# Performance work log

Measured on AMD Instinct MI355X. Metric: run time of the kernel, lower is better.

The kernel has to match this reference:

```python
import jax, jax.numpy as jnp
import numpy as np
import math

PAD = 0
EPS = 1e-5


def _mha(x, ids, num_heads, qw, qb, kw, kb, vw, vb, pw, pb):
    # Faithful vectorization of the per-head Python loop: identical math per head.
    B, S, D = x.shape
    d = D // num_heads
    q = (x @ qw + qb).reshape(B, S, num_heads, d)
    k = (x @ kw + kb).reshape(B, S, num_heads, d)
    v = (x @ vw + vb).reshape(B, S, num_heads, d)
    scores = jnp.einsum('bqhd,bkhd->bhqk', q, k) / math.sqrt(d)
    key_mask = (ids != PAD)[:, None, None, :]  # mask padded KEYS only (as in source)
    scores = jnp.where(key_mask, scores, -jnp.inf)
    w = jax.nn.softmax(scores, axis=-1)
    out = jnp.einsum('bhqk,bkhd->bqhd', w, v).reshape(B, S, D)
    return out @ pw + pb + x  # projection + residual


def setup_inputs() -> dict:
    V, D, B, S = 50257, 1024, 64, 512
    key = jax.random.key(0)
    ks = jax.random.split(key, 24)
    s = 0.02

    def lin(k, din, dout):
        k1, k2 = jax.random.split(k)
        return (jax.random.normal(k1, (din, dout), jnp.float32) * s,
                jax.random.normal(k2, (dout,), jnp.float32) * s)

    x = jax.random.randint(ks[0], (B, S), 0, V, dtype=jnp.int64)
    emb_w = jax.random.normal(ks[1], (V, D), jnp.float32) * s
    pos_w = jax.random.normal(ks[2], (512, D), jnp.float32) * s
    a1_qw, a1_qb = lin(ks[3], D, D)
    a1_kw, a1_kb = lin(ks[4], D, D)
    a1_vw, a1_vb = lin(ks[5], D, D)
    a1_pw, a1_pb = lin(ks[6], D, D)
    a2_qw, a2_qb = lin(ks[7], D, D)
    a2_kw, a2_kb = lin(ks[8], D, D)
    a2_vw, a2_vb = lin(ks[9], D, D)
    a2_pw, a2_pb = lin(ks[10], D, D)
    norm_g = jnp.ones((D,), jnp.float32)
    norm_b = jnp.zeros((D,), jnp.float32)
    lin_w, lin_b = lin(ks[11], D, 1)
    return dict(x=x, emb_w=emb_w, pos_w=pos_w,
                a1_qw=a1_qw, a1_qb=a1_qb, a1_kw=a1_kw, a1_kb=a1_kb,
                a1_vw=a1_vw, a1_vb=a1_vb, a1_pw=a1_pw, a1_pb=a1_pb,
                a2_qw=a2_qw, a2_qb=a2_qb, a2_kw=a2_kw, a2_kb=a2_kb,
                a2_vw=a2_vw, a2_vb=a2_vb, a2_pw=a2_pw, a2_pb=a2_pb,
                norm_g=norm_g, norm_b=norm_b, lin_w=lin_w, lin_b=lin_b)


def reference(x, emb_w, pos_w,
              a1_qw, a1_qb, a1_kw, a1_kb, a1_vw, a1_vb, a1_pw, a1_pb,
              a2_qw, a2_qb, a2_kw, a2_kb, a2_vw, a2_vb, a2_pw, a2_pb,
              norm_g, norm_b, lin_w, lin_b):
    B, S = x.shape
    h = emb_w[x] + pos_w[jnp.arange(S)][None, :, :]  # word + positional emb
    res_emb = h
    h = _mha(h, x, 8, a1_qw, a1_qb, a1_kw, a1_kb, a1_vw, a1_vb, a1_pw, a1_pb)
    # dropout is identity in eval
    h = _mha(h, x, 4, a2_qw, a2_qb, a2_kw, a2_kb, a2_vw, a2_vb, a2_pw, a2_pb)
    h = h + res_emb
    # mean pooling over non-pad tokens (type=0 branch)
    m = (x != PAD)[:, :, None].astype(h.dtype)
    pooled = jnp.sum(h * m, axis=1) / jnp.sum(m, axis=1)
    # LayerNorm
    mu = jnp.mean(pooled, axis=-1, keepdims=True)
    var = jnp.mean((pooled - mu) ** 2, axis=-1, keepdims=True)
    normed = (pooled - mu) / jnp.sqrt(var + EPS) * norm_g + norm_b
    return normed @ lin_w + lin_b  # [B, 1]
```

## Files before the change

kernel.cpp:

```cpp
#include <hip/hip_runtime.h>

typedef unsigned short u16;
typedef short short8 __attribute__((ext_vector_type(8)));
typedef unsigned short u16x8 __attribute__((ext_vector_type(8)));
typedef float f32x4 __attribute__((ext_vector_type(4)));
typedef const __attribute__((address_space(1))) void* gptr_t;
typedef __attribute__((address_space(3))) void* lptr_t;

#define B_  64
#define S_  512
#define D_  1024
#define BS_ (B_*S_)

__device__ __forceinline__ float b2f(u16 v) {
    union { float f; unsigned u; } c; c.u = ((unsigned)v) << 16; return c.f;
}
__device__ __forceinline__ u16 f2b(float f) {
    union { float f; unsigned u; } c; c.f = f;
    unsigned r = c.u + 0x7FFFu + ((c.u >> 16) & 1u);
    return (u16)(r >> 16);
}

__global__ void detect_k(const u16* __restrict__ raw, int* __restrict__ flag) {
    __shared__ int cnt;
    if (threadIdx.x == 0) cnt = 0;
    __syncthreads();
    u16 v = raw[threadIdx.x * 2];
    int e = (v >> 7) & 0xFF;
    int sane = (e >= 64 && e <= 150) ? 1 : 0;
    atomicAdd(&cnt, sane);
    __syncthreads();
    if (threadIdx.x == 0) *flag = (cnt >= 192) ? 1 : 0;
}

__global__ __launch_bounds__(256) void convert_params_k(
    const void* b0, const void* b1, const void* b2, const void* b3,
    const void* b4, const void* b5, const void* b6, const void* b7,
    const void* g, const void* be, const void* lw, const void* lb,
    const int* __restrict__ flagp, u16* __restrict__ dst)
{
    const void* srcs[12] = {b0, b1, b2, b3, b4, b5, b6, b7, g, be, lw, lb};
    int slot = blockIdx.x;
    int n = (slot == 11) ? 1 : 1024;
    int f = *flagp;
    const void* s = srcs[slot];
    for (int i = threadIdx.x; i < n; i += 256) {
        float v = f ? b2f(((const u16*)s)[i]) : ((const float*)s)[i];
        dst[slot * 1024 + i] = f2b(v);
    }
}

__global__ __launch_bounds__(256) void transpose_all_k(
    const void* w0, const void* w1, const void* w2, const void* w3,
    const void* w4, const void* w5, const void* w6, const void* w7,
    u16* __restrict__ WtBase, const int* __restrict__ flagp) {
    __shared__ float t[32][33];
    const void* srcs[8] = {w0, w1, w2, w3, w4, w5, w6, w7};
    int z = blockIdx.z;
    const void* W = srcs[z];
    u16* Wt = WtBase + (size_t)z * (D_ * D_);
    int f = *flagp;
    int tx = threadIdx.x, ty = threadIdx.y;
    int x0 = blockIdx.x * 32, y0 = blockIdx.y * 32;
    for (int i = ty; i < 32; i += 8) {
        size_t idx = (size_t)(y0 + i) * D_ + x0 + tx;
        t[i][tx] = f ? b2f(((const u16*)W)[idx]) : ((const float*)W)[idx];
    }
    __syncthreads();
    for (int i = ty; i < 32; i += 8)
        Wt[(size_t)(x0 + i) * D_ + y0 + tx] = f2b(t[tx][i]);
}

__global__ __launch_bounds__(256) void embed_k(const int* __restrict__ x, const void* __restrict__ emb,
                                               const void* __restrict__ pos, u16* __restrict__ h0,
                                               const int* __restrict__ flagp) {
    int f = *flagp;
    int bs = blockIdx.x;
    int s = bs & (S_ - 1);
    int tok = x[bs];
    u16* orow = h0 + (size_t)bs * D_;
    int c = threadIdx.x * 4;
    float e0, e1, e2, e3, p0, p1, p2, p3;
    if (f) {
        ushort4 e = *(const ushort4*)((const u16*)emb + (size_t)tok * D_ + c);
        ushort4 p = *(const ushort4*)((const u16*)pos + (size_t)s * D_ + c);
        e0 = b2f(e.x); e1 = b2f(e.y); e2 = b2f(e.z); e3 = b2f(e.w);
        p0 = b2f(p.x); p1 = b2f(p.y); p2 = b2f(p.z); p3 = b2f(p.w);
    } else {
        float4 e = *(const float4*)((const float*)emb + (size_t)tok * D_ + c);
        float4 p = *(const float4*)((const float*)pos + (size_t)s * D_ + c);
        e0 = e.x; e1 = e.y; e2 = e.z; e3 = e.w;
        p0 = p.x; p1 = p.y; p2 = p.z; p3 = p.w;
    }
    ushort4 o;
    o.x = f2b(e0 + p0); o.y = f2b(e1 + p1); o.z = f2b(e2 + p2); o.w = f2b(e3 + p3);
    *(ushort4*)(orow + c) = o;
}

template <int NT>
__global__ __launch_bounds__(512, 2) void gemm256_k(
    const u16* __restrict__ A, const u16* __restrict__ Bt,
    const u16* __restrict__ bias,
    const u16* __restrict__ res, const u16* __restrict__ res2,
    u16* __restrict__ Cq, u16* __restrict__ Ck, u16* __restrict__ Vt,
    const int* __restrict__ xm, float* __restrict__ pool)
{
    int bid = blockIdx.x;
    int xcd = bid & 7;
    int loc = bid >> 3;
    int chunk = loc >> 6;
    int r = loc & 63;
    int mt = xcd * 16 + (r >> 2);
    int nt = chunk * 4 + (r & 3);
    int m0 = mt * 256, n0 = nt * 256;

    int tid = threadIdx.x;
    int lane = tid & 63, wid = tid >> 6, quad = lane >> 4, l16 = lane & 15;
    int wm = wid >> 2, wn = wid & 3;
    int pxor = l16 & 7;

    __shared__ __align__(16) u16 lds[2][2][2][128 * 64];

    f32x4 acc[8][4];
#pragma unroll
    for (int i = 0; i < 8; i++)
#pragma unroll
        for (int j = 0; j < 4; j++) acc[i][j] = (f32x4){0.f, 0.f, 0.f, 0.f};

    int srow = tid >> 3;
    int skof = ((tid & 7) ^ (srow & 7)) * 8;

    auto STAGE_HALF = [&](int kt, int mat, int hlf) {
        int p = kt & 1;
        int kbase = kt * 64;
        const u16* src = (mat == 0)
            ? A  + (size_t)(m0 + hlf * 128) * D_ + kbase
            : Bt + (size_t)(n0 + hlf * 128) * D_ + kbase;
        u16* dst = &lds[p][mat][hlf][0];
        __builtin_amdgcn_global_load_lds((gptr_t)(src + (size_t)srow * D_ + skof),
                                         (lptr_t)(dst + tid * 8), 16, 0, 0);
        __builtin_amdgcn_global_load_lds((gptr_t)(src + (size_t)(srow + 64) * D_ + skof),
                                         (lptr_t)(dst + 4096 + tid * 8), 16, 0, 0);
    };

    STAGE_HALF(0, 0, 0); STAGE_HALF(0, 0, 1);
    STAGE_HALF(0, 1, 0); STAGE_HALF(0, 1, 1);
    STAGE_HALF(1, 1, 0); STAGE_HALF(1, 1, 1);
    asm volatile("s_waitcnt vmcnt(4)" ::: "memory");
    __builtin_amdgcn_s_barrier();

    int brow0 = (wn & 1) * 64;
    for (int kt = 0; kt < 16; ++kt) {
        int p = kt & 1;
        const u16* Ah = &lds[p][0][wm][0];
        const u16* Bh = &lds[p][1][wn >> 1][0];
        short8 bf[4][2];
#pragma unroll
        for (int q = 0; q < 4; ++q) {
            if (q == 0) {
#pragma unroll
                for (int nj = 0; nj < 4; ++nj)
#pragma unroll
                    for (int kh = 0; kh < 2; ++kh)
                        bf[nj][kh] = *(const short8*)&Bh[(brow0 + nj * 16 + l16) * 64 +
                                                         ((kh * 4 + quad) ^ pxor) * 8];
            }
            short8 af[2][2];
#pragma unroll
            for (int mi2 = 0; mi2 < 2; ++mi2)
#pragma unroll
                for (int kh = 0; kh < 2; ++kh)
                    af[mi2][kh] = *(const short8*)&Ah[((2 * q + mi2) * 16 + l16) * 64 +
                                                      ((kh * 4 + quad) ^ pxor) * 8];
            if (q == 0 && kt + 1 < 16) STAGE_HALF(kt + 1, 0, 0);
            if (q == 1 && kt + 1 < 16) STAGE_HALF(kt + 1, 0, 1);
            if (q == 2 && kt + 2 < 16) STAGE_HALF(kt + 2, 1, 0);
            if (q == 3 && kt + 2 < 16) STAGE_HALF(kt + 2, 1, 1);
            __builtin_amdgcn_s_barrier();
            asm volatile("s_waitcnt lgkmcnt(0)" ::: "memory");
            __builtin_amdgcn_sched_barrier(0);
            __builtin_amdgcn_s_setprio(1);
#pragma unroll
            for (int kh = 0; kh < 2; ++kh)
#pragma unroll
                for (int mi2 = 0; mi2 < 2; ++mi2)
#pragma unroll
                    for (int nj = 0; nj < 4; ++nj)
                        acc[2 * q + mi2][nj] = __builtin_amdgcn_mfma_f32_16x16x32_bf16(
                            af[mi2][kh], bf[nj][kh], acc[2 * q + mi2][nj], 0, 0, 0);
            __builtin_amdgcn_s_setprio(0);
            __builtin_amdgcn_s_barrier();
        }
        if (kt < 15) {
            if (kt < 14) asm volatile("s_waitcnt vmcnt(4)" ::: "memory");
            else         asm volatile("s_waitcnt vmcnt(0)" ::: "memory");
            __builtin_amdgcn_s_barrier();
        }
    }

    __syncthreads();
    float* fl = (float*)(&lds[0][0][0][0]) + wid * 1104;

    int nbase = n0 + wn * 64;
    bool vwave = (NT == 12) && (nbase >= 2048);

    if (vwave) {
        int colv = nbase + lane - 2048;
        float bv = b2f(bias[nbase + lane]);
#pragma unroll
        for (int mi = 0; mi < 8; ++mi) {
#pragma unroll
            for (int nj = 0; nj < 4; ++nj)
                *(f32x4*)&fl[(nj * 16 + l16) * 17 + quad * 4] = acc[mi][nj];
            asm volatile("s_waitcnt lgkmcnt(0)" ::: "memory");
            int rowbase = m0 + wm * 128 + mi * 16;
            int bb = rowbase >> 9, sb0 = rowbase & (S_ - 1);
            u16x8 o0, o1;
#pragma unroll
            for (int s = 0; s < 8; ++s) {
                o0[s] = f2b(fl[lane * 17 + s] + bv);
                o1[s] = f2b(fl[lane * 17 + 8 + s] + bv);
            }
            u16* dst = Vt + ((size_t)bb * D_ + colv) * S_ + sb0;
            *(u16x8*)dst = o0;
            *(u16x8*)(dst + 8) = o1;
            asm volatile("" ::: "memory");
        }
    } else {
        u16* Cd = (NT == 12 && nbase >= 1024) ? Ck : Cq;
        int rr2 = lane >> 2, sg = lane & 3;
        float bvv[2][8];
#pragma unroll
        for (int g = 0; g < 2; ++g) {
            u16x8 b8 = *(const u16x8*)&bias[nbase + sg * 8 + g * 32];
#pragma unroll
            for (int j = 0; j < 8; ++j) bvv[g][j] = b2f(b8[j]);
        }
        float psum[2][8];
#pragma unroll
        for (int g = 0; g < 2; ++g)
#pragma unroll
            for (int j = 0; j < 8; ++j) psum[g][j] = 0.f;
        int rowb0 = m0 + wm * 128;
        int b_ = rowb0 >> 9;
        const int* xb_ = pool ? (xm + b_ * S_) : nullptr;

#pragma unroll
        for (int mi = 0; mi < 8; ++mi) {
#pragma unroll
            for (int nj = 0; nj < 4; ++nj)
                *(f32x4*)&fl[(nj * 16 + l16) * 17 + quad * 4] = acc[mi][nj];
            asm volatile("s_waitcnt lgkmcnt(0)" ::: "memory");
            int row_g = rowb0 + mi * 16 + rr2;
            int msk = pool ? (xb_[row_g & (S_ - 1)] != 0) : 0;
#pragma unroll
            for (int g = 0; g < 2; ++g) {
                int c0 = sg * 8 + g * 32;
                int colc = (nbase + c0) & 1023;
                size_t idx = (size_t)row_g * D_ + colc;
                float v[8];
#pragma unroll
                for (int j = 0; j < 8; ++j)
                    v[j] = fl[(c0 + j) * 17 + rr2] + bvv[g][j];
                if (res) {
                    u16x8 r8 = *(const u16x8*)&res[idx];
#pragma unroll
                    for (int j = 0; j < 8; ++j) v[j] += b2f(r8[j]);
                }
                if (res2) {
                    u16x8 r8 = *(const u16x8*)&res2[idx];
#pragma unroll
                    for (int j = 0; j < 8; ++j) v[j] += b2f(r8[j]);
                }
                if (pool) {
                    if (msk)
#pragma unroll
                        for (int j = 0; j < 8; ++j) psum[g][j] += v[j];
                } else {
                    u16x8 o;
#pragma unroll
                    for (int j = 0; j < 8; ++j) o[j] = f2b(v[j]);
                    *(u16x8*)&Cd[idx] = o;
                }
            }
            asm volatile("" ::: "memory");
        }
        if (pool) {
#pragma unroll
            for (int g = 0; g < 2; ++g)
#pragma unroll
                for (int j = 0; j < 8; ++j) {
#pragma unroll
                    for (int m = 4; m <= 32; m <<= 1)
                        psum[g][j] += __shfl_xor(psum[g][j], m, 64);
                }
            if (rr2 == 0) {
#pragma unroll
                for (int g = 0; g < 2; ++g) {
                    int colc = (nbase + sg * 8 + g * 32) & 1023;
#pragma unroll
                    for (int j = 0; j < 8; ++j)
                        atomicAdd(&pool[b_ * 1024 + colc + j], psum[g][j]);
                }
            }
        }
    }
}

template <int HD, int NBUF>
__global__ __launch_bounds__(512, HD == 128 ? 4 : 2) void attn8_k(
    const u16* Q, const u16* __restrict__ Kn, const u16* __restrict__ Vt,
    const int* __restrict__ x, u16* O, int H)
{
    constexpr int NKF = HD / 32, NOF = HD / 16;
    constexpr int KP = HD + 8;
    constexpr int VP = (HD == 256 && NBUF == 2) ? 36 : 40;
    constexpr int KC = (32 * HD / 8) / 512;
    constexpr int VC = (HD * 32 / 8) / 512;
    const float scale = (HD == 128) ? 0.08838834764831845f : 0.0625f;
    int bh = blockIdx.x;
    int b = bh / H, h = bh - b * H;
    int tid = threadIdx.x, wid = tid >> 6, lane = tid & 63, quad = lane >> 4, l16 = lane & 15;
    int qrow = blockIdx.y * 128 + wid * 16;

    const u16* Qb = Q + (size_t)(b * S_) * D_ + h * HD;
    const u16* Kb = Kn + (size_t)(b * S_) * D_ + h * HD;
    const u16* Vb = Vt + ((size_t)b * D_ + h * HD) * S_;
    const int* xb = x + b * S_;

    __shared__ __align__(16) u16 Ks[NBUF][32 * KP];
    __shared__ __align__(16) u16 Vs[NBUF][HD * VP];
    __shared__ __align__(16) u16 Pl[8 * 16 * 32];

    short8 qf[NKF];
#pragma unroll
    for (int f = 0; f < NKF; ++f)
        qf[f] = *(const short8*)(Qb + (size_t)(qrow + l16) * D_ + f * 32 + quad * 8);

    f32x4 of[NOF];
    float lpart[4];
#pragma unroll
    for (int f = 0; f < NOF; ++f) of[f] = (f32x4){0.f, 0.f, 0.f, 0.f};
#pragma unroll
    for (int r = 0; r < 4; ++r) lpart[r] = 0.f;

    short8 kreg[KC], vreg[VC];
    auto LOADKV = [&](int key0) {
#pragma unroll
        for (int i = 0; i < KC; ++i) {
            int c = tid + i * 512;
            int row = c / (HD / 8), col = (c % (HD / 8)) * 8;
            kreg[i] = *(const short8*)(Kb + (size_t)(key0 + row) * D_ + col);
        }
#pragma unroll
        for (int i = 0; i < VC; ++i) {
            int c = tid + i * 512;
            int row = c >> 2, col = (c & 3) * 8;
            vreg[i] = *(const short8*)(Vb + (size_t)row * S_ + key0 + col);
        }
    };

    LOADKV(0);

    for (int t = 0; t < 16; ++t) {
        int key0 = t * 32;
        int p = (NBUF == 2) ? (t & 1) : 0;
        if (NBUF == 1) __syncthreads();
#pragma unroll
        for (int i = 0; i < KC; ++i) {
            int c = tid + i * 512;
            int row = c / (HD / 8), col = (c % (HD / 8)) * 8;
            *(short8*)&Ks[p][row * KP + col] = kreg[i];
        }
#pragma unroll
        for (int i = 0; i < VC; ++i) {
            int c = tid + i * 512;
            int row = c >> 2, col = (c & 3) * 8;
            *(short8*)&Vs[p][row * VP + col] = vreg[i];
        }
        if (key0 + 32 < S_) LOADKV(key0 + 32);
        int tok0 = xb[key0 + l16] != 0;
        int tok1 = xb[key0 + 16 + l16] != 0;
        __syncthreads();

        f32x4 sc0 = (f32x4){0.f, 0.f, 0.f, 0.f};
        f32x4 sc1 = (f32x4){0.f, 0.f, 0.f, 0.f};
#pragma unroll
        for (int f = 0; f < NKF; ++f) {
            short8 k0 = *(const short8*)&Ks[p][l16 * KP + f * 32 + quad * 8];
            short8 k1 = *(const short8*)&Ks[p][(16 + l16) * KP + f * 32 + quad * 8];
            sc0 = __builtin_amdgcn_mfma_f32_16x16x32_bf16(qf[f], k0, sc0, 0, 0, 0);
            sc1 = __builtin_amdgcn_mfma_f32_16x16x32_bf16(qf[f], k1, sc1, 0, 0, 0);
        }
#pragma unroll
        for (int r = 0; r < 4; ++r) {
            float p0 = tok0 ? __expf(sc0[r] * scale) : 0.f;
            float p1 = tok1 ? __expf(sc1[r] * scale) : 0.f;
            lpart[r] += p0 + p1;
            Pl[wid * 512 + (quad * 4 + r) * 32 + l16] = f2b(p0);
            Pl[wid * 512 + (quad * 4 + r) * 32 + 16 + l16] = f2b(p1);
        }
        __asm volatile("s_waitcnt lgkmcnt(0)" ::: "memory");
        short8 pf = *(const short8*)&Pl[wid * 512 + l16 * 32 + quad * 8];
#pragma unroll
        for (int f = 0; f < NOF; ++f) {
            short8 vf = *(const short8*)&Vs[p][(f * 16 + l16) * VP + quad * 8];
            of[f] = __builtin_amdgcn_mfma_f32_16x16x32_bf16(pf, vf, of[f], 0, 0, 0);
        }
    }

    u16* Ob = O + (size_t)(b * S_) * D_ + h * HD;
    float rl[4];
#pragma unroll
    for (int r = 0; r < 4; ++r) {
        float l = lpart[r];
#pragma unroll
        for (int msk = 1; msk < 16; msk <<= 1) l += __shfl_xor(l, msk, 64);
        rl[r] = 1.0f / l;
    }
#pragma unroll
    for (int f = 0; f < NOF; ++f)
#pragma unroll
        for (int r = 0; r < 4; ++r)
            Ob[(size_t)(qrow + quad * 4 + r) * D_ + f * 16 + l16] =
                f2b(of[f][r] * rl[r]);
}

__global__ __launch_bounds__(256) void pool_zero_k(float* __restrict__ pooled) {
    int b = blockIdx.x;
    for (int i = threadIdx.x; i < 1024; i += 256) pooled[b * 1024 + i] = 0.f;
}

__global__ __launch_bounds__(256) void pool_final_k(
    const float* __restrict__ pooled, const int* __restrict__ x,
    const u16* __restrict__ prm, void* __restrict__ out, const int* __restrict__ flagp)
{
    __shared__ float sb[8];
    __shared__ int sbi[4];
    const u16* g  = prm + 8 * 1024;
    const u16* be = prm + 9 * 1024;
    const u16* lw = prm + 10 * 1024;
    const u16* lb = prm + 11 * 1024;
    int b = blockIdx.x;
    int c = threadIdx.x * 4;
    int wid = threadIdx.x >> 6, lane = threadIdx.x & 63;

    const int* xb = x + b * S_;
    int localc = 0;
    for (int i = threadIdx.x; i < S_; i += 256) localc += (xb[i] != 0);
#pragma unroll
    for (int m = 32; m >= 1; m >>= 1) localc += __shfl_xor(localc, m, 64);
    if (lane == 0) sbi[wid] = localc;
    __syncthreads();
    int n = sbi[0] + sbi[1] + sbi[2] + sbi[3];

    float inv = 1.0f / (float)(n > 0 ? n : 1);
    float p0 = pooled[b * 1024 + c + 0] * inv;
    float p1 = pooled[b * 1024 + c + 1] * inv;
    float p2 = pooled[b * 1024 + c + 2] * inv;
    float p3 = pooled[b * 1024 + c + 3] * inv;
    float s1 = p0 + p1 + p2 + p3;
    float s2 = p0 * p0 + p1 * p1 + p2 * p2 + p3 * p3;
#pragma unroll
    for (int m = 32; m >= 1; m >>= 1) { s1 += __shfl_xor(s1, m, 64); s2 += __shfl_xor(s2, m, 64); }
    if (lane == 0) { sb[wid] = s1; sb[4 + wid] = s2; }
    __syncthreads();
    float S1 = sb[0] + sb[1] + sb[2] + sb[3];
    float S2 = sb[4] + sb[5] + sb[6] + sb[7];
    float mu = S1 * (1.0f / 1024.0f);
    float var = S2 * (1.0f / 1024.0f) - mu * mu;
    float rstd = rsqrtf(var + 1e-5f);
    float dot = ((p0 - mu) * rstd * b2f(g[c + 0]) + b2f(be[c + 0])) * b2f(lw[c + 0])
              + ((p1 - mu) * rstd * b2f(g[c + 1]) + b2f(be[c + 1])) * b2f(lw[c + 1])
              + ((p2 - mu) * rstd * b2f(g[c + 2]) + b2f(be[c + 2])) * b2f(lw[c + 2])
              + ((p3 - mu) * rstd * b2f(g[c + 3]) + b2f(be[c + 3])) * b2f(lw[c + 3]);
#pragma unroll
    for (int m = 32; m >= 1; m >>= 1) dot += __shfl_xor(dot, m, 64);
    __syncthreads();
    if (lane == 0) sb[wid] = dot;
    __syncthreads();
    if (threadIdx.x == 0) {
        float v = sb[0] + sb[1] + sb[2] + sb[3] + b2f(lb[0]);
        if (*flagp) ((u16*)out)[b] = f2b(v);
        else        ((float*)out)[b] = v;
    }
}

extern "C" void kernel_launch(void* const* d_in, const int* in_sizes, int n_in,
                              void* d_out, int out_size, void* d_ws, size_t ws_size,
                              hipStream_t stream)
{
    (void)in_sizes; (void)n_in; (void)out_size; (void)ws_size;
    const int* x = (const int*)d_in[0];

    char* ws = (char*)d_ws;
    size_t off = 0;
    auto carve = [&](size_t bytes) -> char* {
        char* p = ws + off;
        off += (bytes + 255) & ~(size_t)255;
        return p;
    };
    int* flag    = (int*)carve(256);
    u16* prm     = (u16*)carve(12 * 1024 * 2);
    float* pooled = (float*)carve(64 * 1024 * 4);
    int* cnt     = (int*)carve(64 * 4);
    (void)cnt;
    const size_t WB = (size_t)D_ * D_ * 2;
    const size_t HB = (size_t)BS_ * D_ * 2;
    u16* wt0 = (u16*)carve(WB * 8);
    u16* h0   = (u16*)carve(HB);
    u16* buf2 = (u16*)carve(HB);
    u16* buf3 = (u16*)carve(HB);
    u16* buf4 = (u16*)carve(HB);
    u16* buf5 = (u16*)carve(HB);
    const size_t WE = (size_t)D_ * D_;

    detect_k<<<1, 256, 0, stream>>>((const u16*)d_in[1], flag);
    convert_params_k<<<12, 256, 0, stream>>>(
        d_in[4], d_in[6], d_in[8], d_in[10], d_in[12], d_in[14], d_in[16], d_in[18],
        d_in[19], d_in[20], d_in[21], d_in[22], flag, prm);

    transpose_all_k<<<dim3(32, 32, 8), dim3(32, 8), 0, stream>>>(
        d_in[3], d_in[5], d_in[7], d_in[9], d_in[11], d_in[13], d_in[15], d_in[17],
        wt0, flag);

    embed_k<<<BS_, 256, 0, stream>>>(x, d_in[1], d_in[2], h0, flag);

    pool_zero_k<<<B_, 256, 0, stream>>>(pooled);

    gemm256_k<12><<<1536, 512, 0, stream>>>(h0, wt0 + 0 * WE, prm + 0 * 1024,
                                            nullptr, nullptr, buf2, buf3, buf4,
                                            nullptr, nullptr);
    attn8_k<128, 2><<<dim3(B_ * 8, 4), 512, 0, stream>>>(buf2, buf3, buf4, x, buf2, 8);
    gemm256_k<4><<<512, 512, 0, stream>>>(buf2, wt0 + 3 * WE, prm + 3 * 1024,
                                          h0, nullptr, buf5, nullptr, nullptr,
                                          nullptr, nullptr);
    gemm256_k<12><<<1536, 512, 0, stream>>>(buf5, wt0 + 4 * WE, prm + 4 * 1024,
                                            nullptr, nullptr, buf2, buf3, buf4,
                                            nullptr, nullptr);
    attn8_k<256, 2><<<dim3(B_ * 4, 4), 512, 0, stream>>>(buf2, buf3, buf4, x, buf2, 4);
    gemm256_k<4><<<512, 512, 0, stream>>>(buf2, wt0 + 7 * WE, prm + 7 * 1024,
                                          buf5, h0, nullptr, nullptr, nullptr,
                                          x, pooled);

    pool_final_k<<<B_, 256, 0, stream>>>(pooled, x, prm, d_out, flag);
}
```

Baseline: 974.2 us.

## Add dedicated 128x256-tile QKV GEMM kernel with higher occupancy

Replaces the 256x256-tile QKV projection GEMM with a new kernel that uses 128x256 tiles, a simpler double-buffered K=32 pipeline, 4x4 accumulators per wave, and launch bounds allowing 4 blocks per CU. It launches 3072 blocks in place of 1536, with an XCD-aware tile mapping. The aim is more occupancy and better load balance for the QKV projection, at the cost of less reuse per tile (more global traffic for B). The V-transpose epilogue moves from the generic GEMM into the new kernel, leaving the old GEMM with only the Q/out-projection path.

```diff
diff --git a/kernel.cpp b/kernel.cpp
--- a/kernel.cpp
+++ b/kernel.cpp
@@ -97,6 +97,140 @@
     *(ushort4*)(orow + c) = o;
 }
 
+__global__ __launch_bounds__(512, 4) void gemmqkv_k(
+    const u16* __restrict__ A, const u16* __restrict__ Bt,
+    const u16* __restrict__ bias,
+    u16* __restrict__ Cq, u16* __restrict__ Ck, u16* __restrict__ Vt)
+{
+    int bid = blockIdx.x;
+    int xcd = bid & 7;
+    int loc = bid >> 3;
+    int chunk = loc >> 7;
+    int r = loc & 127;
+    int mt = xcd * 32 + (r >> 2);
+    int nt = chunk * 4 + (r & 3);
+    int m0 = mt * 128, n0 = nt * 256;
+
+    int tid = threadIdx.x;
+    int lane = tid & 63, wid = tid >> 6, quad = lane >> 4, l16 = lane & 15;
+    int wm = wid >> 2, wn = wid & 3;
+    int pxor = (l16 >> 1) & 3;
+
+    __shared__ __align__(16) u16 lds[2][12288];
+
+    f32x4 acc[4][4];
+#pragma unroll
+    for (int i = 0; i < 4; i++)
+#pragma unroll
+        for (int j = 0; j < 4; j++) acc[i][j] = (f32x4){0.f, 0.f, 0.f, 0.f};
+
+    int srow = tid >> 2;
+    int skof = (((tid & 3) ^ ((tid >> 3) & 3)) * 8);
+
+    auto STAGE = [&](int s) {
+        int p = s & 1;
+        int kbase = s * 32;
+        __builtin_amdgcn_global_load_lds(
+            (gptr_t)(A + (size_t)(m0 + srow) * D_ + kbase + skof),
+            (lptr_t)(&lds[p][0] + tid * 8), 16, 0, 0);
+#pragma unroll
+        for (int l = 0; l < 2; ++l) {
+            int row = l * 128 + srow;
+            __builtin_amdgcn_global_load_lds(
+                (gptr_t)(Bt + (size_t)(n0 + row) * D_ + kbase + skof),
+                (lptr_t)(&lds[p][4096] + l * 4096 + tid * 8), 16, 0, 0);
+        }
+    };
+
+    STAGE(0);
+    for (int s = 0; s < 32; ++s) {
+        int p = s & 1;
+        asm volatile("s_waitcnt vmcnt(0)" ::: "memory");
+        __builtin_amdgcn_s_barrier();
+        const u16* Ah = &lds[p][0];
+        const u16* Bh = &lds[p][4096];
+        short8 af[4], bf[4];
+#pragma unroll
+        for (int mi = 0; mi < 4; ++mi)
+            af[mi] = *(const short8*)&Ah[(wm * 64 + mi * 16 + l16) * 32 + ((quad ^ pxor) * 8)];
+#pragma unroll
+        for (int nj = 0; nj < 4; ++nj)
+            bf[nj] = *(const short8*)&Bh[(wn * 64 + nj * 16 + l16) * 32 + ((quad ^ pxor) * 8)];
+        if (s + 1 < 32) STAGE(s + 1);
+        asm volatile("s_waitcnt lgkmcnt(0)" ::: "memory");
+        __builtin_amdgcn_sched_barrier(0);
+        __builtin_amdgcn_s_setprio(1);
+#pragma unroll
+        for (int mi = 0; mi < 4; ++mi)
+#pragma unroll
+            for (int nj = 0; nj < 4; ++nj)
+                acc[mi][nj] = __builtin_amdgcn_mfma_f32_16x16x32_bf16(
+                    af[mi], bf[nj], acc[mi][nj], 0, 0, 0);
+        __builtin_amdgcn_s_setprio(0);
+    }
+
+    __syncthreads();
+    float* fl = (float*)(&lds[0][0]) + wid * 1104;
+
+    int nbase = n0 + wn * 64;
+    int rowb0 = m0 + wm * 64;
+    bool vwave = (nbase >= 2048);
+
+    if (vwave) {
+        int colv = nbase + lane - 2048;
+        float bv = b2f(bias[nbase + lane]);
+#pragma unroll
+        for (int mi = 0; mi < 4; ++mi) {
+#pragma unroll
+            for (int nj = 0; nj < 4; ++nj)
+                *(f32x4*)&fl[(nj * 16 + l16) * 17 + quad * 4] = acc[mi][nj];
+            asm volatile("s_waitcnt lgkmcnt(0)" ::: "memory");
+            int rowbase = rowb0 + mi * 16;
+            int bb = rowbase >> 9, sb0 = rowbase & (S_ - 1);
+            u16x8 o0, o1;
+#pragma unroll
+            for (int s = 0; s < 8; ++s) {
+                o0[s] = f2b(fl[lane * 17 + s] + bv);
+                o1[s] = f2b(fl[lane * 17 + 8 + s] + bv);
+            }
+            u16* dst = Vt + ((size_t)bb * D_ + colv) * S_ + sb0;
+            *(u16x8*)dst = o0;
+            *(u16x8*)(dst + 8) = o1;
+            asm volatile("" ::: "memory");
+        }
+    } else {
+        u16* Cd = (nbase >= 1024) ? Ck : Cq;
+        int rr2 = lane >> 2, sg = lane & 3;
+        float bvv[2][8];
+#pragma unroll
+        for (int g = 0; g < 2; ++g) {
+            u16x8 b8 = *(const u16x8*)&bias[nbase + sg * 8 + g * 32];
+#pragma unroll
+            for (int j = 0; j < 8; ++j) bvv[g][j] = b2f(b8[j]);
+        }
+#pragma unroll
+        for (int mi = 0; mi < 4; ++mi) {
+#pragma unroll
+            for (int nj = 0; nj < 4; ++nj)
+                *(f32x4*)&fl[(nj * 16 + l16) * 17 + quad * 4] = acc[mi][nj];
+            asm volatile("s_waitcnt lgkmcnt(0)" ::: "memory");
+            int row_g = rowb0 + mi * 16 + rr2;
+#pragma unroll
+            for (int g = 0; g < 2; ++g) {
+                int c0 = sg * 8 + g * 32;
+                int colc = (nbase + c0) & 1023;
+                size_t idx = (size_t)row_g * D_ + colc;
+                u16x8 o;
+#pragma unroll
+                for (int j = 0; j < 8; ++j)
+                    o[j] = f2b(fl[(c0 + j) * 17 + rr2] + bvv[g][j]);
+                *(u16x8*)&Cd[idx] = o;
+            }
+            asm volatile("" ::: "memory");
+        }
+    }
+}
+
 template <int NT>
 __global__ __launch_bounds__(512, 2) void gemm256_k(
     const u16* __restrict__ A, const u16* __restrict__ Bt,
@@ -202,32 +336,8 @@
     float* fl = (float*)(&lds[0][0][0][0]) + wid * 1104;
 
     int nbase = n0 + wn * 64;
-    bool vwave = (NT == 12) && (nbase >= 2048);
-
-    if (vwave) {
-        int colv = nbase + lane - 2048;
-        float bv = b2f(bias[nbase + lane]);
-#pragma unroll
-        for (int mi = 0; mi < 8; ++mi) {
-#pragma unroll
-            for (int nj = 0; nj < 4; ++nj)
-                *(f32x4*)&fl[(nj * 16 + l16) * 17 + quad * 4] = acc[mi][nj];
-            asm volatile("s_waitcnt lgkmcnt(0)" ::: "memory");
-            int rowbase = m0 + wm * 128 + mi * 16;
-            int bb = rowbase >> 9, sb0 = rowbase & (S_ - 1);
-            u16x8 o0, o1;
-#pragma unroll
-            for (int s = 0; s < 8; ++s) {
-                o0[s] = f2b(fl[lane * 17 + s] + bv);
-                o1[s] = f2b(fl[lane * 17 + 8 + s] + bv);
-            }
-            u16* dst = Vt + ((size_t)bb * D_ + colv) * S_ + sb0;
-            *(u16x8*)dst = o0;
-            *(u16x8*)(dst + 8) = o1;
-            asm volatile("" ::: "memory");
-        }
-    } else {
-        u16* Cd = (NT == 12 && nbase >= 1024) ? Ck : Cq;
+    {
+        u16* Cd = Cq;
         int rr2 = lane >> 2, sg = lane & 3;
         float bvv[2][8];
 #pragma unroll
@@ -305,6 +415,7 @@
             }
         }
     }
+    (void)Ck; (void)Vt;
 }
 
 template <int HD, int NBUF>
@@ -503,8 +614,6 @@
     int* flag    = (int*)carve(256);
     u16* prm     = (u16*)carve(12 * 1024 * 2);
     float* pooled = (float*)carve(64 * 1024 * 4);
-    int* cnt     = (int*)carve(64 * 4);
-    (void)cnt;
     const size_t WB = (size_t)D_ * D_ * 2;
     const size_t HB = (size_t)BS_ * D_ * 2;
     u16* wt0 = (u16*)carve(WB * 8);
@@ -528,16 +637,14 @@
 
     pool_zero_k<<<B_, 256, 0, stream>>>(pooled);
 
-    gemm256_k<12><<<1536, 512, 0, stream>>>(h0, wt0 + 0 * WE, prm + 0 * 1024,
-                                            nullptr, nullptr, buf2, buf3, buf4,
-                                            nullptr, nullptr);
+    gemmqkv_k<<<3072, 512, 0, stream>>>(h0, wt0 + 0 * WE, prm + 0 * 1024,
+                                        buf2, buf3, buf4);
     attn8_k<128, 2><<<dim3(B_ * 8, 4), 512, 0, stream>>>(buf2, buf3, buf4, x, buf2, 8);
     gemm256_k<4><<<512, 512, 0, stream>>>(buf2, wt0 + 3 * WE, prm + 3 * 1024,
                                           h0, nullptr, buf5, nullptr, nullptr,
                                           nullptr, nullptr);
-    gemm256_k<12><<<1536, 512, 0, stream>>>(buf5, wt0 + 4 * WE, prm + 4 * 1024,
-                                            nullptr, nullptr, buf2, buf3, buf4,
-                                            nullptr, nullptr);
+    gemmqkv_k<<<3072, 512, 0, stream>>>(buf5, wt0 + 4 * WE, prm + 4 * 1024,
+                                        buf2, buf3, buf4);
     attn8_k<256, 2><<<dim3(B_ * 4, 4), 512, 0, stream>>>(buf2, buf3, buf4, x, buf2, 4);
     gemm256_k<4><<<512, 512, 0, stream>>>(buf2, wt0 + 7 * WE, prm + 7 * 1024,
                                           buf5, h0, nullptr, nullptr, nullptr,
```

Result: slower. 998.7 us (+2.5%).
